# Kernel optimization log

Hardware: AMD Instinct MI355X
Metric: run time of the kernel (lower is better)

The kernel has to match this reference:

```python
import jax, jax.numpy as jnp
from jax import lax
import numpy as np

B, C, H, W = 16, 32, 256, 256
K = 3  # kernel size, padding=1 -> SAME


def setup_inputs() -> dict:
    key = jax.random.key(0)
    k1, k2, k3, k4, k5, k6 = jax.random.split(key, 6)
    x = jax.random.normal(k1, (B, C, H, W), dtype=jnp.float32)
    gate_values = jax.random.uniform(k2, (B, C), dtype=jnp.float32)
    # Stacked per-output-channel Conv2d experts == one [C, C, K, K] conv (OIHW)
    fan_in = C * K * K
    bound = 1.0 / np.sqrt(fan_in)
    w1 = jax.random.uniform(k3, (C, C, K, K), minval=-bound, maxval=bound, dtype=jnp.float32)
    b1 = jax.random.uniform(k4, (C,), minval=-bound, maxval=bound, dtype=jnp.float32)
    w2 = jax.random.uniform(k5, (C, C, K, K), minval=-bound, maxval=bound, dtype=jnp.float32)
    b2 = jax.random.uniform(k6, (C,), minval=-bound, maxval=bound, dtype=jnp.float32)
    return {"x": x, "gate_values": gate_values, "w1": w1, "b1": b1, "w2": w2, "b2": b2}


def _moe_conv(x, w, b, g):
    # x: [B,C,H,W], w: [C,C,K,K] (OIHW), b: [C], g: [B,C] effective gate
    y = lax.conv_general_dilated(
        x, w, window_strides=(1, 1), padding='SAME',
        dimension_numbers=('NCHW', 'OIHW', 'NCHW'))
    y = y + b[None, :, None, None]
    return y * g[:, :, None, None]


def reference(x, gate_values, w1, b1, w2, b2):
    # gate rows with value <= 0 are never written -> output stays zero;
    # selected rows are multiplied by the gate value (bias included).
    g = gate_values * (gate_values > 0).astype(gate_values.dtype)
    h = jax.nn.relu(_moe_conv(x, w1, b1, g))
    h = jax.nn.relu(_moe_conv(h, w2, b2, g))
    return h + x
```

## Files before the change

kernel.cpp:

```cpp
#include <hip/hip_runtime.h>

#define BB 16
#define CC 32
#define HH 256
#define WW 256

#define TW 32
#define TH 8
#define CIP 36

typedef short bf16x8 __attribute__((ext_vector_type(8)));
typedef float f32x16 __attribute__((ext_vector_type(16)));

struct alignas(8)  U2 { unsigned x, y; };
struct alignas(16) U4 { U2 lo, hi; };

__device__ __forceinline__ unsigned short f2bf(float f) {
    unsigned u = __float_as_uint(f);
    u += 0x7fffu + ((u >> 16) & 1u);
    return (unsigned short)(u >> 16);
}

__global__ void wprep(const float* __restrict__ w1, const float* __restrict__ w2,
                      unsigned short* __restrict__ wq) {
    int idx = blockIdx.x * 256 + threadIdx.x;
    if (idx >= 18 * 2 * 32 * 8) return;
    int j    = idx & 7;
    int n    = (idx >> 3) & 31;
    int half = (idx >> 8) & 1;
    int st   = idx >> 9;
    int s = st & 1, pos = st >> 1;
    int ci = s * 16 + half * 8 + j;
    int src = (n * CC + ci) * 9 + pos;
    wq[idx]        = f2bf(w1[src]);
    wq[9216 + idx] = f2bf(w2[src]);
}

template<bool FIRST>
__global__ __launch_bounds__(256)
void conv_mfma(const void* __restrict__ in,
               const unsigned short* __restrict__ wq,
               const float* __restrict__ bias,
               const float* __restrict__ gate,
               const float* __restrict__ resid,
               void* __restrict__ out)
{
    __shared__ unsigned short xs[TH + 2][TW + 2][CIP];
    __shared__ float gs[CC], bs[CC];

    const int t  = threadIdx.x;
    const int b  = blockIdx.z;
    const int y0 = blockIdx.y * TH;
    const int x0 = blockIdx.x * TW;

    if (t < CC) {
        float gv = gate[b * CC + t];
        gs[t] = gv > 0.f ? gv : 0.f;
        bs[t] = bias[t];
    }

    const int lane = t & 63;
    const int wv   = t >> 6;
    const int col  = lane & 31;
    const int half = lane >> 5;

    bf16x8 wf[18];
    #pragma unroll
    for (int st = 0; st < 18; ++st) {
        U4 w = ((const U4*)wq)[(st * 2 + half) * 32 + col];
        wf[st] = __builtin_bit_cast(bf16x8, w);
    }

    if (FIRST) {
        const float* x = (const float*)in;
        for (int idx = t; idx < CC * (TH + 2) * (TW + 2); idx += 256) {
            int ci  = idx / ((TH + 2) * (TW + 2));
            int rem = idx - ci * ((TH + 2) * (TW + 2));
            int y   = rem / (TW + 2);
            int xx  = rem - y * (TW + 2);
            int gy = y0 + y - 1, gx = x0 + xx - 1;
            float v = 0.f;
            if (gy >= 0 && gy < HH && gx >= 0 && gx < WW)
                v = x[(((size_t)b * CC + ci) * HH + gy) * WW + gx];
            xs[y][xx][ci] = f2bf(v);
        }
    } else {
        const unsigned short* h = (const unsigned short*)in;
        for (int idx = t; idx < (TH + 2) * (TW + 2) * 4; idx += 256) {
            int q = idx & 3;
            int p = idx >> 2;
            int y  = p / (TW + 2);
            int xx = p - y * (TW + 2);
            int gy = y0 + y - 1, gx = x0 + xx - 1;
            U4 v; v.lo = {0u, 0u}; v.hi = {0u, 0u};
            if (gy >= 0 && gy < HH && gx >= 0 && gx < WW)
                v = *(const U4*)(h + (((size_t)b * HH + gy) * WW + gx) * CC + q * 8);
            *(U2*)&xs[y][xx][q * 8]     = v.lo;
            *(U2*)&xs[y][xx][q * 8 + 4] = v.hi;
        }
    }
    __syncthreads();

    f32x16 acc0 = {0,0,0,0,0,0,0,0,0,0,0,0,0,0,0,0};
    f32x16 acc1 = {0,0,0,0,0,0,0,0,0,0,0,0,0,0,0,0};
    const int r0 = wv * 2, r1 = wv * 2 + 1;

    #pragma unroll
    for (int st = 0; st < 18; ++st) {
        const int pos = st >> 1, s = st & 1;
        const int kh = pos / 3, kw = pos - kh * 3;
        const int ci0 = s * 16 + half * 8;
        U4 xa, xb;
        xa.lo = *(const U2*)&xs[r0 + kh][col + kw][ci0];
        xa.hi = *(const U2*)&xs[r0 + kh][col + kw][ci0 + 4];
        xb.lo = *(const U2*)&xs[r1 + kh][col + kw][ci0];
        xb.hi = *(const U2*)&xs[r1 + kh][col + kw][ci0 + 4];
        acc0 = __builtin_amdgcn_mfma_f32_32x32x16_bf16(wf[st], __builtin_bit_cast(bf16x8, xa), acc0, 0, 0, 0);
        acc1 = __builtin_amdgcn_mfma_f32_32x32x16_bf16(wf[st], __builtin_bit_cast(bf16x8, xb), acc1, 0, 0, 0);
    }

    if (FIRST) {
        unsigned short* o = (unsigned short*)out;
        size_t p0 = (((size_t)b * HH + y0 + r0) * WW + x0 + col) * CC;
        size_t p1 = (((size_t)b * HH + y0 + r1) * WW + x0 + col) * CC;
        #pragma unroll
        for (int reg = 0; reg < 16; ++reg) {
            int co = (reg & 3) + 8 * (reg >> 2) + 4 * half;
            float v0 = (acc0[reg] + bs[co]) * gs[co]; v0 = v0 > 0.f ? v0 : 0.f;
            float v1 = (acc1[reg] + bs[co]) * gs[co]; v1 = v1 > 0.f ? v1 : 0.f;
            o[p0 + co] = f2bf(v0);
            o[p1 + co] = f2bf(v1);
        }
    } else {
        float* o = (float*)out;
        #pragma unroll
        for (int reg = 0; reg < 16; ++reg) {
            int co = (reg & 3) + 8 * (reg >> 2) + 4 * half;
            size_t i0 = (((size_t)b * CC + co) * HH + y0 + r0) * WW + x0 + col;
            size_t i1 = (((size_t)b * CC + co) * HH + y0 + r1) * WW + x0 + col;
            float v0 = (acc0[reg] + bs[co]) * gs[co];
            float v1 = (acc1[reg] + bs[co]) * gs[co];
            o[i0] = fmaxf(v0, 0.f) + resid[i0];
            o[i1] = fmaxf(v1, 0.f) + resid[i1];
        }
    }
}

extern "C" void kernel_launch(void* const* d_in, const int* in_sizes, int n_in,
                              void* d_out, int out_size, void* d_ws, size_t ws_size,
                              hipStream_t stream) {
    const float* x  = (const float*)d_in[0];
    const float* gv = (const float*)d_in[1];
    const float* w1 = (const float*)d_in[2];
    const float* b1 = (const float*)d_in[3];
    const float* w2 = (const float*)d_in[4];
    const float* b2 = (const float*)d_in[5];
    float* out = (float*)d_out;

    unsigned short* h1 = (unsigned short*)d_ws;
    unsigned short* wq = h1 + (size_t)BB * HH * WW * CC;

    wprep<<<36, 256, 0, stream>>>(w1, w2, wq);

    dim3 grid(WW / TW, HH / TH, BB);
    conv_mfma<true ><<<grid, 256, 0, stream>>>(x,  wq,        b1, gv, nullptr, h1);
    conv_mfma<false><<<grid, 256, 0, stream>>>(h1, wq + 9216, b2, gv, x,       out);
}
```

Measured before the change: 380.1 us.

## Split input channels into two LDS passes and vectorize bf16 output stores

The conv kernel now processes the 32 input channels in two 16-channel chunks. It reuses a smaller LDS tile (CIP 20) and loads only 9 weight fragments per chunk, which cuts LDS footprint and register pressure and should allow more resident blocks. The FP32 input load for the first conv is restructured so that each warp reads contiguous x-columns, with the halo columns loaded separately and divisions removed. The first conv's bf16 output writes are packed into 8-byte stores. The cost is an extra __syncthreads per block and a serialized load-compute pass per chunk.

```diff
diff --git a/kernel.cpp b/kernel.cpp
--- a/kernel.cpp
+++ b/kernel.cpp
@@ -7,7 +7,7 @@
 
 #define TW 32
 #define TH 8
-#define CIP 36
+#define CIP 20
 
 typedef short bf16x8 __attribute__((ext_vector_type(8)));
 typedef float f32x16 __attribute__((ext_vector_type(16)));
@@ -29,8 +29,8 @@
     int n    = (idx >> 3) & 31;
     int half = (idx >> 8) & 1;
     int st   = idx >> 9;
-    int s = st & 1, pos = st >> 1;
-    int ci = s * 16 + half * 8 + j;
+    int c = st & 1, pos = st >> 1;
+    int ci = c * 16 + half * 8 + j;
     int src = (n * CC + ci) * 9 + pos;
     wq[idx]        = f2bf(w1[src]);
     wq[9216 + idx] = f2bf(w2[src]);
@@ -61,83 +61,126 @@
 
     const int lane = t & 63;
     const int wv   = t >> 6;
-    const int col  = lane & 31;
+    const int n    = lane & 31;
     const int half = lane >> 5;
-
-    bf16x8 wf[18];
-    #pragma unroll
-    for (int st = 0; st < 18; ++st) {
-        U4 w = ((const U4*)wq)[(st * 2 + half) * 32 + col];
-        wf[st] = __builtin_bit_cast(bf16x8, w);
-    }
-
-    if (FIRST) {
-        const float* x = (const float*)in;
-        for (int idx = t; idx < CC * (TH + 2) * (TW + 2); idx += 256) {
-            int ci  = idx / ((TH + 2) * (TW + 2));
-            int rem = idx - ci * ((TH + 2) * (TW + 2));
-            int y   = rem / (TW + 2);
-            int xx  = rem - y * (TW + 2);
-            int gy = y0 + y - 1, gx = x0 + xx - 1;
-            float v = 0.f;
-            if (gy >= 0 && gy < HH && gx >= 0 && gx < WW)
-                v = x[(((size_t)b * CC + ci) * HH + gy) * WW + gx];
-            xs[y][xx][ci] = f2bf(v);
-        }
-    } else {
-        const unsigned short* h = (const unsigned short*)in;
-        for (int idx = t; idx < (TH + 2) * (TW + 2) * 4; idx += 256) {
-            int q = idx & 3;
-            int p = idx >> 2;
-            int y  = p / (TW + 2);
-            int xx = p - y * (TW + 2);
-            int gy = y0 + y - 1, gx = x0 + xx - 1;
-            U4 v; v.lo = {0u, 0u}; v.hi = {0u, 0u};
-            if (gy >= 0 && gy < HH && gx >= 0 && gx < WW)
-                v = *(const U4*)(h + (((size_t)b * HH + gy) * WW + gx) * CC + q * 8);
-            *(U2*)&xs[y][xx][q * 8]     = v.lo;
-            *(U2*)&xs[y][xx][q * 8 + 4] = v.hi;
-        }
-    }
-    __syncthreads();
+    const int r0 = wv * 2, r1 = wv * 2 + 1;
 
     f32x16 acc0 = {0,0,0,0,0,0,0,0,0,0,0,0,0,0,0,0};
     f32x16 acc1 = {0,0,0,0,0,0,0,0,0,0,0,0,0,0,0,0};
-    const int r0 = wv * 2, r1 = wv * 2 + 1;
 
     #pragma unroll
-    for (int st = 0; st < 18; ++st) {
-        const int pos = st >> 1, s = st & 1;
-        const int kh = pos / 3, kw = pos - kh * 3;
-        const int ci0 = s * 16 + half * 8;
-        U4 xa, xb;
-        xa.lo = *(const U2*)&xs[r0 + kh][col + kw][ci0];
-        xa.hi = *(const U2*)&xs[r0 + kh][col + kw][ci0 + 4];
-        xb.lo = *(const U2*)&xs[r1 + kh][col + kw][ci0];
-        xb.hi = *(const U2*)&xs[r1 + kh][col + kw][ci0 + 4];
-        acc0 = __builtin_amdgcn_mfma_f32_32x32x16_bf16(wf[st], __builtin_bit_cast(bf16x8, xa), acc0, 0, 0, 0);
-        acc1 = __builtin_amdgcn_mfma_f32_32x32x16_bf16(wf[st], __builtin_bit_cast(bf16x8, xb), acc1, 0, 0, 0);
+    for (int c = 0; c < 2; ++c) {
+        if (c) __syncthreads();
+
+        bf16x8 wf[9];
+        #pragma unroll
+        for (int pos = 0; pos < 9; ++pos) {
+            U4 w = ((const U4*)wq)[((pos * 2 + c) * 2 + half) * 32 + n];
+            wf[pos] = __builtin_bit_cast(bf16x8, w);
+        }
+
+        if (FIRST) {
+            const float* x = (const float*)in;
+            const size_t basep = ((size_t)b * CC + c * 16) * HH;
+            {
+                const int xcM = 1 + (t & 31);
+                const int g   = t >> 5;
+                const int gx  = x0 + (t & 31);
+                #pragma unroll
+                for (int i = 0; i < 20; ++i) {
+                    int p  = g + 8 * i;
+                    int y  = p >> 4;
+                    int ci = p & 15;
+                    int gy = y0 + y - 1;
+                    float v = 0.f;
+                    if ((unsigned)gy < HH)
+                        v = x[(basep + (size_t)ci * HH + gy) * WW + gx];
+                    xs[y][xcM][ci] = f2bf(v);
+                }
+            }
+            if (t < 64) {
+                int side = t & 1;
+                int r    = t >> 1;
+                int xc   = side ? 33 : 0;
+                int gx   = side ? (x0 + 32) : (x0 - 1);
+                bool xok = (unsigned)gx < WW;
+                #pragma unroll
+                for (int i = 0; i < 5; ++i) {
+                    int p  = r + 32 * i;
+                    int y  = p >> 4;
+                    int ci = p & 15;
+                    int gy = y0 + y - 1;
+                    float v = 0.f;
+                    if (xok && (unsigned)gy < HH)
+                        v = x[(basep + (size_t)ci * HH + gy) * WW + gx];
+                    xs[y][xc][ci] = f2bf(v);
+                }
+            }
+        } else {
+            const unsigned short* h = (const unsigned short*)in;
+            #pragma unroll
+            for (int i = 0; i < 3; ++i) {
+                int idx = t + 256 * i;
+                if (idx < 680) {
+                    int q   = idx & 1;
+                    int pix = idx >> 1;
+                    int y   = pix / 34;
+                    int xc  = pix - y * 34;
+                    int gy = y0 + y - 1, gx = x0 + xc - 1;
+                    U4 v; v.lo = {0u, 0u}; v.hi = {0u, 0u};
+                    if ((unsigned)gy < HH && (unsigned)gx < WW)
+                        v = *(const U4*)(h + (((size_t)b * HH + gy) * WW + gx) * CC + c * 16 + q * 8);
+                    *(U2*)&xs[y][xc][q * 8]     = v.lo;
+                    *(U2*)&xs[y][xc][q * 8 + 4] = v.hi;
+                }
+            }
+        }
+        __syncthreads();
+
+        #pragma unroll
+        for (int pos = 0; pos < 9; ++pos) {
+            const int kh = pos / 3, kw = pos - kh * 3;
+            const unsigned short* pa = &xs[r0 + kh][n + kw][half * 8];
+            const unsigned short* pb = &xs[r1 + kh][n + kw][half * 8];
+            U4 xa, xb;
+            xa.lo = *(const U2*)pa;       xa.hi = *(const U2*)(pa + 4);
+            xb.lo = *(const U2*)pb;       xb.hi = *(const U2*)(pb + 4);
+            acc0 = __builtin_amdgcn_mfma_f32_32x32x16_bf16(wf[pos], __builtin_bit_cast(bf16x8, xa), acc0, 0, 0, 0);
+            acc1 = __builtin_amdgcn_mfma_f32_32x32x16_bf16(wf[pos], __builtin_bit_cast(bf16x8, xb), acc1, 0, 0, 0);
+        }
     }
 
     if (FIRST) {
         unsigned short* o = (unsigned short*)out;
-        size_t p0 = (((size_t)b * HH + y0 + r0) * WW + x0 + col) * CC;
-        size_t p1 = (((size_t)b * HH + y0 + r1) * WW + x0 + col) * CC;
+        size_t p0 = (((size_t)b * HH + y0 + r0) * WW + x0 + n) * CC;
+        size_t p1 = (((size_t)b * HH + y0 + r1) * WW + x0 + n) * CC;
+        #pragma unroll
+        for (int q = 0; q < 4; ++q) {
+            unsigned short a0[4], a1[4];
+            #pragma unroll
+            for (int r = 0; r < 4; ++r) {
+                int reg = q * 4 + r;
+                int co  = r + 8 * q + 4 * half;
+                float u0 = (acc0[reg] + bs[co]) * gs[co];
+                float u1 = (acc1[reg] + bs[co]) * gs[co];
+                a0[r] = f2bf(fmaxf(u0, 0.f));
+                a1[r] = f2bf(fmaxf(u1, 0.f));
+            }
+            U2 w0, w1;
+            w0.x = (unsigned)a0[0] | ((unsigned)a0[1] << 16);
+            w0.y = (unsigned)a0[2] | ((unsigned)a0[3] << 16);
+            w1.x = (unsigned)a1[0] | ((unsigned)a1[1] << 16);
+            w1.y = (unsigned)a1[2] | ((unsigned)a1[3] << 16);
+            *(U2*)(o + p0 + q * 8 + half * 4) = w0;
+            *(U2*)(o + p1 + q * 8 + half * 4) = w1;
+        }
+    } else {
+        float* o = (float*)out;
         #pragma unroll
         for (int reg = 0; reg < 16; ++reg) {
             int co = (reg & 3) + 8 * (reg >> 2) + 4 * half;
-            float v0 = (acc0[reg] + bs[co]) * gs[co]; v0 = v0 > 0.f ? v0 : 0.f;
-            float v1 = (acc1[reg] + bs[co]) * gs[co]; v1 = v1 > 0.f ? v1 : 0.f;
-            o[p0 + co] = f2bf(v0);
-            o[p1 + co] = f2bf(v1);
-        }
-    } else {
-        float* o = (float*)out;
-        #pragma unroll
-        for (int reg = 0; reg < 16; ++reg) {
-            int co = (reg & 3) + 8 * (reg >> 2) + 4 * half;
-            size_t i0 = (((size_t)b * CC + co) * HH + y0 + r0) * WW + x0 + col;
-            size_t i1 = (((size_t)b * CC + co) * HH + y0 + r1) * WW + x0 + col;
+            size_t i0 = (((size_t)b * CC + co) * HH + y0 + r0) * WW + x0 + n;
+            size_t i1 = (((size_t)b * CC + co) * HH + y0 + r1) * WW + x0 + n;
             float v0 = (acc0[reg] + bs[co]) * gs[co];
             float v1 = (acc1[reg] + bs[co]) * gs[co];
             o[i0] = fmaxf(v0, 0.f) + resid[i0];
```

Measured after the change: 414.8 us. 1.09x slower.
